# Performance work log

Measured on AMD Instinct MI355X. Metric: run time of the kernel, lower is better.

Reference implementation:

```python
import jax, jax.numpy as jnp
import numpy as np

N_OPCODES = 31
B, S, D = 64, 16, 1024
MAX_STEPS = 16


def setup_inputs() -> dict:
    key = jax.random.key(0)
    k1, k2, k3, k4 = jax.random.split(key, 4)
    return {
        "opcode_logits": jax.random.normal(k1, (B, S, N_OPCODES), dtype=jnp.float32),
        "operands": jax.random.normal(k2, (B, S, 4), dtype=jnp.float32),
        "signal": jax.random.normal(k3, (B, D), dtype=jnp.float32),
        "op_kernels": jax.random.normal(k4, (N_OPCODES, D, D), dtype=jnp.float32) * 0.01,
    }


def reference(opcode_logits, operands, signal, op_kernels):
    # opcode_logits: (B,S,O), operands: (B,S,4), signal: (B,D), op_kernels: (O,D,D)
    n_steps = min(opcode_logits.shape[1], MAX_STEPS)
    weights = jax.nn.softmax(opcode_logits, axis=-1)  # (B,S,O)

    # time-major inputs for scan: (n_steps, B, O) and (n_steps, B, 1)
    ws = jnp.swapaxes(weights[:, :n_steps], 0, 1)
    gate_logits = jnp.swapaxes(operands[:, :n_steps, 3:4], 0, 1)

    def step(h, inputs):
        w, gl = inputs  # (B,O), (B,1)
        gate = jax.nn.sigmoid(gl)
        # equivalent to h @ (sum_o w_o K_o) but never forms the (B,D,D) kernel
        transformed = jnp.einsum('bo,bd,odk->bk', w, h, op_kernels)
        h_new = gate * transformed + (1.0 - gate) * h
        return h_new, None

    h, _ = jax.lax.scan(step, signal, (ws, gate_logits))
    return h
```

## Files before the change

kernel.cpp:

```cpp
#include <hip/hip_runtime.h>
#include <cstddef>
#include <cstdint>

#define NB 64
#define ND 1024
#define NO 31
#define NSTEPS 16
#define KS 62
#define KT32 992

typedef _Float16 half8 __attribute__((ext_vector_type(8)));
typedef float floatx4 __attribute__((ext_vector_type(4)));

__global__ void softmax_k(const float* __restrict__ logits, float* __restrict__ W) {
    int row = blockIdx.x * blockDim.x + threadIdx.x;
    if (row >= NB * NSTEPS) return;
    const float* x = logits + (size_t)row * NO;
    float m = -1e30f;
    for (int o = 0; o < NO; ++o) m = fmaxf(m, x[o]);
    float e[NO]; float s = 0.f;
    for (int o = 0; o < NO; ++o) { e[o] = expf(x[o] - m); s += e[o]; }
    float inv = 1.0f / s;
    float* wo = W + (size_t)row * NO;
    for (int o = 0; o < NO; ++o) wo[o] = e[o] * inv;
}

__global__ void init16_k(const float* __restrict__ h, _Float16* __restrict__ h16) {
    int u = blockIdx.x * 256 + threadIdx.x;
    int d8 = u >> 6, b = u & 63;
    const float* src = h + (size_t)b * ND + d8 * 8;
    half8 v;
    #pragma unroll
    for (int j = 0; j < 8; ++j) v[j] = (_Float16)src[j];
    *(half8*)(h16 + (size_t)u * 8) = v;
}

__global__ __launch_bounds__(256) void kconv_k(const float* __restrict__ K,
                                               _Float16* __restrict__ Ktf) {
    __shared__ float tile[32 * 256];
    int kt  = blockIdx.x >> 2;
    int nb4 = blockIdx.x & 3;
    int tid = threadIdx.x;
    int lane = tid & 63, w = tid >> 6;

    {
        const float* src = K + ((size_t)kt * 32) * ND + nb4 * 256;
        #pragma unroll
        for (int i = 0; i < 8; ++i) {
            int r = i * 4 + w;
            int x = lane * 4;
            int xs = x ^ (((r >> 3) & 1) << 4);
            float4 v = *(const float4*)(src + (size_t)r * ND + x);
            *(float4*)&tile[r * 256 + xs] = v;
        }
    }
    __syncthreads();

    int kl0 = (lane >> 4) * 8;
    int swz = ((lane >> 4) & 1) << 4;
    #pragma unroll
    for (int i = 0; i < 4; ++i) {
        int ns_local = i * 4 + w;
        int nl = ns_local * 16 + (lane & 15);
        int xsw = nl ^ swz;
        half8 v;
        #pragma unroll
        for (int j = 0; j < 8; ++j) v[j] = (_Float16)tile[(kl0 + j) * 256 + xsw];
        int ns = nb4 * 16 + ns_local;
        size_t unit = ((size_t)ns * KT32 + kt) * 64 + lane;
        *(half8*)(Ktf + unit * 8) = v;
    }
}

__global__ __launch_bounds__(256) void gemm_k(
    const _Float16* __restrict__ h16, const _Float16* __restrict__ Ktf,
    const float* __restrict__ W, float* __restrict__ P, int step)
{
    __shared__ _Float16 lds_a[64 * 512];
    int nb = blockIdx.x;
    int ks = blockIdx.y;
    int tid = threadIdx.x;
    int l = tid & 63, w = tid >> 6;
    int o = ks >> 1;
    int ml = l & 15, q = l >> 4;
    int ns0 = nb * 8 + w * 2;

    const half8* bp0 = (const half8*)Ktf + ((size_t)(ns0 + 0) * KT32 + (size_t)ks * 16) * 64 + l;
    const half8* bp1 = (const half8*)Ktf + ((size_t)(ns0 + 1) * KT32 + (size_t)ks * 16) * 64 + l;
    half8 c00 = bp0[0], c10 = bp1[0];
    half8 c01 = bp0[64], c11 = bp1[64];

    {
        const half8* hg = (const half8*)h16 + (size_t)(ks & 1) * 4096;
        #pragma unroll
        for (int i = 0; i < 16; ++i) {
            int u = i * 256 + tid;
            *(half8*)&lds_a[(size_t)u * 8] = hg[u];
        }
    }
    __syncthreads();

    const half8* Ap = (const half8*)lds_a;
    floatx4 acc[2][4] = {};
    #pragma unroll
    for (int s = 0; s < 16; ++s) {
        half8 f0, f1;
        if (s < 14) {
            f0 = bp0[(size_t)(s + 2) * 64];
            f1 = bp1[(size_t)(s + 2) * 64];
        }
        int abase = (s * 4 + q) * 64 + ml;
        half8 a0 = Ap[abase];
        half8 a1 = Ap[abase + 16];
        half8 a2 = Ap[abase + 32];
        half8 a3 = Ap[abase + 48];
        acc[0][0] = __builtin_amdgcn_mfma_f32_16x16x32_f16(a0, c00, acc[0][0], 0, 0, 0);
        acc[0][1] = __builtin_amdgcn_mfma_f32_16x16x32_f16(a1, c00, acc[0][1], 0, 0, 0);
        acc[0][2] = __builtin_amdgcn_mfma_f32_16x16x32_f16(a2, c00, acc[0][2], 0, 0, 0);
        acc[0][3] = __builtin_amdgcn_mfma_f32_16x16x32_f16(a3, c00, acc[0][3], 0, 0, 0);
        acc[1][0] = __builtin_amdgcn_mfma_f32_16x16x32_f16(a0, c10, acc[1][0], 0, 0, 0);
        acc[1][1] = __builtin_amdgcn_mfma_f32_16x16x32_f16(a1, c10, acc[1][1], 0, 0, 0);
        acc[1][2] = __builtin_amdgcn_mfma_f32_16x16x32_f16(a2, c10, acc[1][2], 0, 0, 0);
        acc[1][3] = __builtin_amdgcn_mfma_f32_16x16x32_f16(a3, c10, acc[1][3], 0, 0, 0);
        if (s < 15) { c00 = c01; c10 = c11; }
        if (s < 14) { c01 = f0; c11 = f1; }
    }

    float wtab[16];
    #pragma unroll
    for (int mt = 0; mt < 4; ++mt)
        #pragma unroll
        for (int r = 0; r < 4; ++r) {
            int b = mt * 16 + q * 4 + r;
            wtab[mt * 4 + r] = W[((size_t)b * NSTEPS + step) * NO + o];
        }
    float* Pks = P + (size_t)ks * (NB * ND);
    #pragma unroll
    for (int tt = 0; tt < 2; ++tt) {
        int n = (ns0 + tt) * 16 + ml;
        #pragma unroll
        for (int mt = 0; mt < 4; ++mt) {
            #pragma unroll
            for (int r = 0; r < 4; ++r) {
                int b = mt * 16 + q * 4 + r;
                Pks[(size_t)b * ND + n] = acc[tt][mt][r] * wtab[mt * 4 + r];
            }
        }
    }
}

__global__ void update_k(const float* __restrict__ hin, const float* __restrict__ P,
                         const float* __restrict__ operands, float* __restrict__ hout,
                         _Float16* __restrict__ h16n, int step)
{
    __shared__ float red[256];
    int tid = threadIdx.x;
    int w = tid >> 6, lane = tid & 63;
    int j = (w & 1) * 64 + lane;
    int g = blockIdx.x * 128 + j;
    const float* p = P + (size_t)((w >> 1) * 31) * (NB * ND) + g;
    float s = 0.f;
    #pragma unroll
    for (int i = 0; i < 31; ++i) s += p[(size_t)i * (NB * ND)];
    red[(w >> 1) * 128 + j] = s;
    __syncthreads();
    if (tid < 128) {
        float tot = red[tid] + red[tid + 128];
        int g2 = blockIdx.x * 128 + tid;
        int b = g2 >> 10, n = g2 & 1023;
        float gl = operands[((size_t)b * NSTEPS + step) * 4 + 3];
        float gt = 1.0f / (1.0f + expf(-gl));
        float val = gt * tot + (1.0f - gt) * hin[g2];
        hout[g2] = val;
        h16n[((size_t)(n >> 3) * 64 + b) * 8 + (n & 7)] = (_Float16)val;
    }
}

extern "C" void kernel_launch(void* const* d_in, const int* in_sizes, int n_in,
                              void* d_out, int out_size, void* d_ws, size_t ws_size,
                              hipStream_t stream)
{
    const float* logits   = (const float*)d_in[0];
    const float* operands = (const float*)d_in[1];
    const float* signal   = (const float*)d_in[2];
    const float* opk      = (const float*)d_in[3];
    float* out = (float*)d_out;
    char* ws = (char*)d_ws;

    size_t offW   = 0;
    size_t offP   = 131072;
    size_t offH   = offP + (size_t)KS * NB * ND * 4;
    size_t offH16 = offH + 2ull * NB * ND * 4;
    size_t offK   = offH16 + 2ull * NB * ND * 2;

    float*    W    = (float*)(ws + offW);
    float*    P    = (float*)(ws + offP);
    float*    h0   = (float*)(ws + offH);
    float*    h1   = h0 + NB * ND;
    _Float16* h16a = (_Float16*)(ws + offH16);
    _Float16* h16b = h16a + NB * ND;
    _Float16* Ktf  = (_Float16*)(ws + offK);

    softmax_k<<<dim3(4), 256, 0, stream>>>(logits, W);
    init16_k<<<dim3(32), 256, 0, stream>>>(signal, h16a);
    kconv_k<<<dim3(3968), 256, 0, stream>>>(opk, Ktf);

    const float* hc = signal;
    float* hn = h0;
    _Float16* h16c = h16a;
    _Float16* h16n = h16b;
    for (int t = 0; t < NSTEPS; ++t) {
        gemm_k<<<dim3(8, KS), 256, 0, stream>>>(h16c, Ktf, W, P, t);
        float* dst = (t == NSTEPS - 1) ? out : hn;
        update_k<<<dim3(512), 256, 0, stream>>>(hc, P, operands, dst, h16n, t);
        hc = dst;
        hn = (hn == h0) ? h1 : h0;
        _Float16* tmp = h16c; h16c = h16n; h16n = tmp;
    }
}
```

Measured before the change: 491.7 us.

## Halve GEMM split-K partials and merge softmax with half-cast init kernel

Each GEMM block now processes a full opcode's K range (two 512-wide halves staged through LDS in turn) instead of half, cutting the split-K count from 62 to 31. This halves the partial-sum buffer writes and the reads in the update kernel, at the cost of half as many blocks (248) and an extra LDS reload and barrier per block. The softmax and fp16-init kernels are also merged into one launch to save one kernel launch.

```diff
diff --git a/kernel.cpp b/kernel.cpp
--- a/kernel.cpp
+++ b/kernel.cpp
@@ -6,33 +6,35 @@
 #define ND 1024
 #define NO 31
 #define NSTEPS 16
-#define KS 62
+#define KS 31
 #define KT32 992
 
 typedef _Float16 half8 __attribute__((ext_vector_type(8)));
 typedef float floatx4 __attribute__((ext_vector_type(4)));
 
-__global__ void softmax_k(const float* __restrict__ logits, float* __restrict__ W) {
-    int row = blockIdx.x * blockDim.x + threadIdx.x;
-    if (row >= NB * NSTEPS) return;
-    const float* x = logits + (size_t)row * NO;
-    float m = -1e30f;
-    for (int o = 0; o < NO; ++o) m = fmaxf(m, x[o]);
-    float e[NO]; float s = 0.f;
-    for (int o = 0; o < NO; ++o) { e[o] = expf(x[o] - m); s += e[o]; }
-    float inv = 1.0f / s;
-    float* wo = W + (size_t)row * NO;
-    for (int o = 0; o < NO; ++o) wo[o] = e[o] * inv;
-}
-
-__global__ void init16_k(const float* __restrict__ h, _Float16* __restrict__ h16) {
-    int u = blockIdx.x * 256 + threadIdx.x;
-    int d8 = u >> 6, b = u & 63;
-    const float* src = h + (size_t)b * ND + d8 * 8;
-    half8 v;
-    #pragma unroll
-    for (int j = 0; j < 8; ++j) v[j] = (_Float16)src[j];
-    *(half8*)(h16 + (size_t)u * 8) = v;
+__global__ void prep_k(const float* __restrict__ logits, float* __restrict__ W,
+                       const float* __restrict__ signal, _Float16* __restrict__ h16) {
+    int bid = blockIdx.x;
+    int tid = threadIdx.x;
+    if (bid < 32) {
+        int u = bid * 256 + tid;
+        int d8 = u >> 6, b = u & 63;
+        const float* src = signal + (size_t)b * ND + d8 * 8;
+        half8 v;
+        #pragma unroll
+        for (int j = 0; j < 8; ++j) v[j] = (_Float16)src[j];
+        *(half8*)(h16 + (size_t)u * 8) = v;
+    } else {
+        int row = (bid - 32) * 256 + tid;
+        const float* x = logits + (size_t)row * NO;
+        float m = -1e30f;
+        for (int o = 0; o < NO; ++o) m = fmaxf(m, x[o]);
+        float e[NO]; float s = 0.f;
+        for (int o = 0; o < NO; ++o) { e[o] = expf(x[o] - m); s += e[o]; }
+        float inv = 1.0f / s;
+        float* wo = W + (size_t)row * NO;
+        for (int o = 0; o < NO; ++o) wo[o] = e[o] * inv;
+    }
 }
 
 __global__ __launch_bounds__(256) void kconv_k(const float* __restrict__ K,
@@ -78,52 +80,57 @@
 {
     __shared__ _Float16 lds_a[64 * 512];
     int nb = blockIdx.x;
-    int ks = blockIdx.y;
+    int o  = blockIdx.y;
     int tid = threadIdx.x;
     int l = tid & 63, w = tid >> 6;
-    int o = ks >> 1;
     int ml = l & 15, q = l >> 4;
     int ns0 = nb * 8 + w * 2;
 
-    const half8* bp0 = (const half8*)Ktf + ((size_t)(ns0 + 0) * KT32 + (size_t)ks * 16) * 64 + l;
-    const half8* bp1 = (const half8*)Ktf + ((size_t)(ns0 + 1) * KT32 + (size_t)ks * 16) * 64 + l;
+    const half8* bp0 = (const half8*)Ktf + ((size_t)(ns0 + 0) * KT32 + (size_t)o * 32) * 64 + l;
+    const half8* bp1 = (const half8*)Ktf + ((size_t)(ns0 + 1) * KT32 + (size_t)o * 32) * 64 + l;
     half8 c00 = bp0[0], c10 = bp1[0];
     half8 c01 = bp0[64], c11 = bp1[64];
 
-    {
-        const half8* hg = (const half8*)h16 + (size_t)(ks & 1) * 4096;
-        #pragma unroll
-        for (int i = 0; i < 16; ++i) {
-            int u = i * 256 + tid;
-            *(half8*)&lds_a[(size_t)u * 8] = hg[u];
-        }
-    }
-    __syncthreads();
-
-    const half8* Ap = (const half8*)lds_a;
     floatx4 acc[2][4] = {};
-    #pragma unroll
-    for (int s = 0; s < 16; ++s) {
-        half8 f0, f1;
-        if (s < 14) {
-            f0 = bp0[(size_t)(s + 2) * 64];
-            f1 = bp1[(size_t)(s + 2) * 64];
-        }
-        int abase = (s * 4 + q) * 64 + ml;
-        half8 a0 = Ap[abase];
-        half8 a1 = Ap[abase + 16];
-        half8 a2 = Ap[abase + 32];
-        half8 a3 = Ap[abase + 48];
-        acc[0][0] = __builtin_amdgcn_mfma_f32_16x16x32_f16(a0, c00, acc[0][0], 0, 0, 0);
-        acc[0][1] = __builtin_amdgcn_mfma_f32_16x16x32_f16(a1, c00, acc[0][1], 0, 0, 0);
-        acc[0][2] = __builtin_amdgcn_mfma_f32_16x16x32_f16(a2, c00, acc[0][2], 0, 0, 0);
-        acc[0][3] = __builtin_amdgcn_mfma_f32_16x16x32_f16(a3, c00, acc[0][3], 0, 0, 0);
-        acc[1][0] = __builtin_amdgcn_mfma_f32_16x16x32_f16(a0, c10, acc[1][0], 0, 0, 0);
-        acc[1][1] = __builtin_amdgcn_mfma_f32_16x16x32_f16(a1, c10, acc[1][1], 0, 0, 0);
-        acc[1][2] = __builtin_amdgcn_mfma_f32_16x16x32_f16(a2, c10, acc[1][2], 0, 0, 0);
-        acc[1][3] = __builtin_amdgcn_mfma_f32_16x16x32_f16(a3, c10, acc[1][3], 0, 0, 0);
-        if (s < 15) { c00 = c01; c10 = c11; }
-        if (s < 14) { c01 = f0; c11 = f1; }
+
+    #pragma unroll
+    for (int p2 = 0; p2 < 2; ++p2) {
+        if (p2) __syncthreads();
+        {
+            const half8* hg = (const half8*)h16 + (size_t)p2 * 4096;
+            #pragma unroll
+            for (int i = 0; i < 16; ++i) {
+                int u = i * 256 + tid;
+                *(half8*)&lds_a[(size_t)u * 8] = hg[u];
+            }
+        }
+        __syncthreads();
+
+        const half8* Ap = (const half8*)lds_a;
+        #pragma unroll
+        for (int s = 0; s < 16; ++s) {
+            int gs = p2 * 16 + s;
+            half8 f0, f1;
+            if (gs < 30) {
+                f0 = bp0[(size_t)(gs + 2) * 64];
+                f1 = bp1[(size_t)(gs + 2) * 64];
+            }
+            int abase = (s * 4 + q) * 64 + ml;
+            half8 a0 = Ap[abase];
+            half8 a1 = Ap[abase + 16];
+            half8 a2 = Ap[abase + 32];
+            half8 a3 = Ap[abase + 48];
+            acc[0][0] = __builtin_amdgcn_mfma_f32_16x16x32_f16(a0, c00, acc[0][0], 0, 0, 0);
+            acc[0][1] = __builtin_amdgcn_mfma_f32_16x16x32_f16(a1, c00, acc[0][1], 0, 0, 0);
+            acc[0][2] = __builtin_amdgcn_mfma_f32_16x16x32_f16(a2, c00, acc[0][2], 0, 0, 0);
+            acc[0][3] = __builtin_amdgcn_mfma_f32_16x16x32_f16(a3, c00, acc[0][3], 0, 0, 0);
+            acc[1][0] = __builtin_amdgcn_mfma_f32_16x16x32_f16(a0, c10, acc[1][0], 0, 0, 0);
+            acc[1][1] = __builtin_amdgcn_mfma_f32_16x16x32_f16(a1, c10, acc[1][1], 0, 0, 0);
+            acc[1][2] = __builtin_amdgcn_mfma_f32_16x16x32_f16(a2, c10, acc[1][2], 0, 0, 0);
+            acc[1][3] = __builtin_amdgcn_mfma_f32_16x16x32_f16(a3, c10, acc[1][3], 0, 0, 0);
+            if (gs < 31) { c00 = c01; c10 = c11; }
+            if (gs < 30) { c01 = f0; c11 = f1; }
+        }
     }
 
     float wtab[16];
@@ -134,7 +141,7 @@
             int b = mt * 16 + q * 4 + r;
             wtab[mt * 4 + r] = W[((size_t)b * NSTEPS + step) * NO + o];
         }
-    float* Pks = P + (size_t)ks * (NB * ND);
+    float* Po = P + (size_t)o * (NB * ND);
     #pragma unroll
     for (int tt = 0; tt < 2; ++tt) {
         int n = (ns0 + tt) * 16 + ml;
@@ -143,7 +150,7 @@
             #pragma unroll
             for (int r = 0; r < 4; ++r) {
                 int b = mt * 16 + q * 4 + r;
-                Pks[(size_t)b * ND + n] = acc[tt][mt][r] * wtab[mt * 4 + r];
+                Po[(size_t)b * ND + n] = acc[tt][mt][r] * wtab[mt * 4 + r];
             }
         }
     }
@@ -156,13 +163,19 @@
     __shared__ float red[256];
     int tid = threadIdx.x;
     int w = tid >> 6, lane = tid & 63;
+    int half = w >> 1;
     int j = (w & 1) * 64 + lane;
     int g = blockIdx.x * 128 + j;
-    const float* p = P + (size_t)((w >> 1) * 31) * (NB * ND) + g;
+    const float* p = P + (size_t)(half * 16) * (NB * ND) + g;
     float s = 0.f;
-    #pragma unroll
-    for (int i = 0; i < 31; ++i) s += p[(size_t)i * (NB * ND)];
-    red[(w >> 1) * 128 + j] = s;
+    if (half == 0) {
+        #pragma unroll
+        for (int i = 0; i < 16; ++i) s += p[(size_t)i * (NB * ND)];
+    } else {
+        #pragma unroll
+        for (int i = 0; i < 15; ++i) s += p[(size_t)i * (NB * ND)];
+    }
+    red[half * 128 + j] = s;
     __syncthreads();
     if (tid < 128) {
         float tot = red[tid] + red[tid + 128];
@@ -201,8 +214,7 @@
     _Float16* h16b = h16a + NB * ND;
     _Float16* Ktf  = (_Float16*)(ws + offK);
 
-    softmax_k<<<dim3(4), 256, 0, stream>>>(logits, W);
-    init16_k<<<dim3(32), 256, 0, stream>>>(signal, h16a);
+    prep_k<<<dim3(36), 256, 0, stream>>>(logits, W, signal, h16a);
     kconv_k<<<dim3(3968), 256, 0, stream>>>(opk, Ktf);
 
     const float* hc = signal;
```

Result: slower. 559.3 us (+13.7%).
